# Kernel optimization log

Hardware: AMD Instinct MI355X
Metric: run time of the kernel (lower is better)

The kernel has to match this reference:

```python
import jax, jax.numpy as jnp
import numpy as np
from jax.tree_util import tree_map

B, T, D = 2, 4096, 1024
C = 512            # chunk_size
P = 16             # n_persistent
H = 2048           # neural-memory hidden
FFN = 4 * D        # ffn_mult * d_model
LR, BETA, ALPHA = 0.01, 0.9, 0.01   # memory lr / momentum / decay
EPS_LN = 1e-5


def _l2norm(x):
    n = jnp.sqrt(jnp.sum(x * x, axis=-1, keepdims=True))
    return x / jnp.maximum(n, 1e-12)


def _ln(x, g, b):
    m = jnp.mean(x, axis=-1, keepdims=True)
    v = jnp.mean((x - m) ** 2, axis=-1, keepdims=True)
    return (x - m) * jax.lax.rsqrt(v + EPS_LN) * g + b


def _mem_mlp(mem, x):
    h = jax.nn.silu(x @ mem['w0'] + mem['b0'])
    return h @ mem['w1'] + mem['b1']


def setup_inputs() -> dict:
    key = jax.random.key(0)
    ks = iter(jax.random.split(key, 32))
    w = lambda *s: jax.random.normal(next(ks), s, jnp.float32) * 0.02
    return dict(
        x=jax.random.normal(next(ks), (B, T, D), jnp.float32),
        wq_ctx=w(D, D), wq=w(D, D), wk=w(D, D), wv=w(D, D),
        w_attn_out=w(D, D), w_gate=w(D, D),
        gate_g=jnp.ones(D), gate_b=jnp.zeros(D),
        n1_g=jnp.ones(D), n1_b=jnp.zeros(D),
        n2_g=jnp.ones(D), n2_b=jnp.zeros(D),
        ffn_w1=w(D, FFN), ffn_b1=jnp.zeros(FFN),
        ffn_w2=w(FFN, D), ffn_b2=jnp.zeros(D),
        pers=w(P, D),
        mem_w0=w(D, H), mem_b0=jnp.zeros(H),
        mem_w1=w(H, D), mem_b1=jnp.zeros(D),
        mem_wk=w(D, D), mem_wv=w(D, D),
    )


def reference(x, wq_ctx, wq, wk, wv, w_attn_out, w_gate, gate_g, gate_b,
              n1_g, n1_b, n2_g, n2_b, ffn_w1, ffn_b1, ffn_w2, ffn_b2,
              pers, mem_w0, mem_b0, mem_w1, mem_b1, mem_wk, mem_wv):
    Bv, Tv, Dv = x.shape
    n_chunks = Tv // C
    scale = Dv ** 0.5
    S = P + 2 * C   # persistent + retrieved-memory tokens + segment
    # prefix-aware causal mask: i attends to j if j < P (persistent prefix) or j <= i
    ii = jnp.arange(S)[:, None]
    jj = jnp.arange(S)[None, :]
    mask = (jj < P) | (jj <= ii)                      # (S, S)

    mem0 = dict(w0=mem_w0, b0=mem_b0, w1=mem_w1, b1=mem_b1)
    mom0 = tree_map(jnp.zeros_like, mem0)

    def attn(seq):                                    # cosine causal attention, single head
        q = _l2norm(seq @ wq) * scale
        k = _l2norm(seq @ wk)
        v = seq @ wv
        scores = jnp.einsum('bqd,bkd->bqk', q, k)
        scores = jnp.where(mask, scores, -jnp.inf)
        a = jax.nn.softmax(scores, axis=-1)
        return jnp.einsum('bqk,bkd->bqd', a, v) @ w_attn_out

    def step(carry, seg):                             # seg: (B, C, D)
        mem, mom = carry
        h = _mem_mlp(mem, _l2norm(seg @ wq_ctx))      # memory retrieval, (B, C, D)
        aug = jnp.concatenate(
            [jnp.broadcast_to(pers, (Bv, P, Dv)), h, seg], axis=1)  # (B, S, D)
        y_aug = aug + attn(_ln(aug, n1_g, n1_b))
        y_t = y_aug[:, P + C:, :]                     # strip persistent, keep last C

        # surprise-gradient memory update with momentum + decay
        kk = y_t @ mem_wk
        vv = y_t @ mem_wv
        loss = lambda m: 0.5 * jnp.sum((_mem_mlp(m, kk) - vv) ** 2) / (Bv * C)
        g = jax.grad(loss)(mem)
        mom = tree_map(lambda m_, g_: BETA * m_ + g_, mom, g)
        mem = tree_map(lambda p_, m_: (1.0 - ALPHA) * p_ - LR * m_, mem, mom)

        mem_out = _mem_mlp(mem, _l2norm(y_t @ wq_ctx))
        gate = jax.nn.sigmoid(_ln(y_t, gate_g, gate_b) @ w_gate)
        o = y_t * gate + mem_out * (1.0 - gate)
        h2 = _ln(o, n2_g, n2_b)
        o = o + (jax.nn.silu(h2 @ ffn_w1 + ffn_b1) @ ffn_w2 + ffn_b2)
        return (mem, mom), o

    x_chunks = x.reshape(Bv, n_chunks, C, Dv).transpose(1, 0, 2, 3)
    _, outs = jax.lax.scan(step, (mem0, mom0), x_chunks)   # (n_chunks, B, C, D)
    return outs.transpose(1, 0, 2, 3).reshape(Bv, Tv, Dv)
```

## Files before the change

### kernel.cpp

```cpp
#include <hip/hip_runtime.h>

#define DD 1024
#define HH 2048
#define TT 4096
#define CC 512
#define PPc 16
#define SB 1040
#define KA 1088
#define FFd 4096
#define NCH 8

typedef _Float16 f16x8 __attribute__((ext_vector_type(8)));
typedef float f32x4 __attribute__((ext_vector_type(4)));

typedef const __attribute__((address_space(1))) _Float16* gas_t;
typedef __attribute__((address_space(3))) _Float16* las_t;

__device__ __forceinline__ void async_cp16(const _Float16* g, _Float16* l) {
    __builtin_amdgcn_global_load_lds((gas_t)g, (las_t)l, 16, 0, 0);
}

template<int N> __device__ __forceinline__ void waitvm() {
    static_assert(N == 0 || N == 2 || N == 3 || N == 4 || N == 6 || N == 8, "unsupported vmcnt");
    if constexpr (N == 0)      asm volatile("s_waitcnt vmcnt(0)" ::: "memory");
    else if constexpr (N == 2) asm volatile("s_waitcnt vmcnt(2)" ::: "memory");
    else if constexpr (N == 3) asm volatile("s_waitcnt vmcnt(3)" ::: "memory");
    else if constexpr (N == 4) asm volatile("s_waitcnt vmcnt(4)" ::: "memory");
    else if constexpr (N == 6) asm volatile("s_waitcnt vmcnt(6)" ::: "memory");
    else                       asm volatile("s_waitcnt vmcnt(8)" ::: "memory");
}
#define BARRIER() asm volatile("s_barrier" ::: "memory")

struct GP {
    const _Float16* A; long bsA, ldA;
    const _Float16* Bt; long bsB, ldB;
    const float* bias;
    const float* resid; long ldr, bsR;
    const float* aux;   long ldx, bsX;
    float* Cf; long ldc, bsC;
    _Float16* Ch; long ldh, bsH;
    _Float16* Ct; long ldt, bsT;
    float* Mom;
    float* Cf2;
    float s1, s2;
    int M, N, K, act;
};

template<int BM, int BN>
__global__ __launch_bounds__(256) void gemm16(GP g)
{
    constexpr int WM = BM / 2, WN = BN / 2;
    constexpr int FA = WM / 16, FB = WN / 16;
    constexpr int LA = BM / 32, LB = BN / 32;
    constexpr int LL = LA + LB;
    constexpr int APAN = BM * 64, BPAN = BN * 64;
    constexpr int NB = 3;
    __shared__ _Float16 smem[NB * (APAN + BPAN)];
    const int tid = threadIdx.x;

    const int gx = gridDim.x, gy = gridDim.y;
    const int nwg = gx * gy * (int)gridDim.z;
    const int orig = ((int)blockIdx.z * gy + (int)blockIdx.y) * gx + (int)blockIdx.x;
    const int xcd = orig & 7, loc = orig >> 3;
    const int q8 = nwg >> 3, r8 = nwg & 7;
    const int lid = (xcd < r8 ? xcd * (q8 + 1) : r8 * (q8 + 1) + (xcd - r8) * q8) + loc;
    const int bxi = lid % gx;
    const int rem = lid / gx;
    const int byi = rem % gy;
    const int z = rem / gy;

    const int K = g.K;
    const long ldA = g.ldA, ldB = g.ldB;
    const int m0 = byi * BM, n0 = bxi * BN;
    const _Float16* Ab = g.A + (long)z * g.bsA + (long)m0 * ldA;
    const _Float16* Bb = g.Bt + (long)z * g.bsB + (long)n0 * ldB;
    const int wave = tid >> 6, lane = tid & 63;
    const int wr = wave >> 1, wc = wave & 1;
    const int fr = lane & 15, kq = lane >> 4;
    const int srow = tid >> 3;
    const int sc8 = (((tid & 7) ^ (srow & 7)) << 3);
    f32x4 acc[FA][FB] = {};

    auto stage = [&](int q, int kk) {
#pragma unroll
        for (int r = 0; r < LA; ++r)
            async_cp16(Ab + (long)(r * 32 + srow) * ldA + kk + sc8,
                       &smem[q * APAN + r * 2048 + wave * 512]);
#pragma unroll
        for (int r = 0; r < LB; ++r)
            async_cp16(Bb + (long)(r * 32 + srow) * ldB + kk + sc8,
                       &smem[NB * APAN + q * BPAN + r * 2048 + wave * 512]);
    };

    const int sl0 = ((kq ^ (fr & 7)) << 3);
    const int sl1 = (((4 + kq) ^ (fr & 7)) << 3);

    auto compute = [&](int q) {
        f16x8 af[2][FA], bf[2][FB];
        const int abase = q * APAN;
#pragma unroll
        for (int i = 0; i < FA; ++i) {
            const int ro = (wr * WM + i * 16 + fr) * 64;
            af[0][i] = *(const f16x8*)&smem[abase + ro + sl0];
            af[1][i] = *(const f16x8*)&smem[abase + ro + sl1];
        }
        const int bbase = NB * APAN + q * BPAN;
#pragma unroll
        for (int j = 0; j < FB; ++j) {
            const int ro = (wc * WN + j * 16 + fr) * 64;
            bf[0][j] = *(const f16x8*)&smem[bbase + ro + sl0];
            bf[1][j] = *(const f16x8*)&smem[bbase + ro + sl1];
        }
        __builtin_amdgcn_s_setprio(1);
#pragma unroll
        for (int h = 0; h < 2; ++h)
#pragma unroll
            for (int i = 0; i < FA; ++i)
#pragma unroll
                for (int j = 0; j < FB; ++j)
                    acc[i][j] = __builtin_amdgcn_mfma_f32_16x16x32_f16(af[h][i], bf[h][j], acc[i][j], 0, 0, 0);
        __builtin_amdgcn_s_setprio(0);
    };

    const int nk = K >> 6;
    stage(0, 0); stage(1, 64);
    int qc = 0, qs = 2;
    for (int t = 0; t < nk; ++t) {
        if (t + 1 < nk) waitvm<LL>(); else waitvm<0>();
        BARRIER();
        if (t + 2 < nk) stage(qs, (t + 2) << 6);
        compute(qc);
        qc = (qc == NB - 1) ? 0 : qc + 1;
        qs = (qs == NB - 1) ? 0 : qs + 1;
    }

#pragma unroll
    for (int i = 0; i < FA; ++i) {
        const int gm0 = m0 + wr * WM + i * 16 + kq * 4;
#pragma unroll
        for (int j = 0; j < FB; ++j) {
            const int gn = n0 + wc * WN + j * 16 + fr;
            if (gn >= g.N) continue;
            if (g.act == 4) {
                const int seg = gn >> 10, gl = gn & 1023;
#pragma unroll
                for (int r = 0; r < 4; ++r) {
                    const int gm = gm0 + r;
                    if (gm >= g.M) continue;
                    const float v = acc[i][j][r];
                    if (seg == 0) g.Ch[(long)gm * 1024 + gl] = (_Float16)v;
                    else if (seg == 1) g.Cf[(long)gm * 1024 + gl] = v;
                    else g.Cf2[(long)gm * 1024 + gl] = v;
                }
            } else {
                const float bv = g.bias ? g.bias[gn] : 0.f;
#pragma unroll
                for (int r = 0; r < 4; ++r) {
                    const int gm = gm0 + r;
                    if (gm >= g.M) continue;
                    const float raw = acc[i][j][r] + bv;
                    float av = raw;
                    if (g.act == 1) av = raw / (1.f + __expf(-raw));
                    else if (g.act == 2) {
                        const float a = g.aux[(long)z * g.bsX + (long)gm * g.ldx + gn];
                        const float s = 1.f / (1.f + __expf(-a));
                        av = raw * (s * (1.f + a * (1.f - s)));
                    }
                    float v = g.s1 * av;
                    if (g.resid) v += g.s2 * g.resid[(long)z * g.bsR + (long)gm * g.ldr + gn];
                    if (g.Cf) g.Cf[(long)z * g.bsC + (long)gm * g.ldc + gn] = (g.act == 1) ? raw : v;
                    if (g.Ch) g.Ch[(long)z * g.bsH + (long)gm * g.ldh + gn] = (_Float16)v;
                    acc[i][j][r] = v;
                }
            }
        }
    }

    if (g.Ct && (g.act != 4 || n0 < 1024)) {
        constexpr int TP = BM + 8;
        __syncthreads();
#pragma unroll
        for (int i = 0; i < FA; ++i) {
            const int lm = wr * WM + i * 16 + kq * 4;
#pragma unroll
            for (int j = 0; j < FB; ++j) {
                const int ln = wc * WN + j * 16 + fr;
#pragma unroll
                for (int r = 0; r < 4; ++r)
                    smem[ln * TP + lm + r] = (_Float16)acc[i][j][r];
            }
        }
        __syncthreads();
        constexpr int TPC = 256 / BN;
        constexpr int SEG = BM / TPC;
        const int ln = tid / TPC, part = tid % TPC;
        const int gn = n0 + ln;
        if (gn < g.N) {
            const int gmb = m0 + part * SEG;
            _Float16* dst = g.Ct + (long)z * g.bsT + (long)gn * g.ldt + gmb;
            const _Float16* src = &smem[ln * TP + part * SEG];
#pragma unroll
            for (int gi = 0; gi < SEG / 8; ++gi)
                if (gmb + gi * 8 < g.M)
                    *(uint4*)(dst + gi * 8) = *(const uint4*)(src + gi * 8);
        }
    }
}

__global__ void momupT_k(const float* __restrict__ dW1, float* __restrict__ mom1,
                         float* __restrict__ w1m, _Float16* __restrict__ w1row,
                         _Float16* __restrict__ w1t,
                         const float* __restrict__ dW0, float* __restrict__ mom0,
                         float* __restrict__ w0m, _Float16* __restrict__ w0t)
{
    __shared__ _Float16 t[64][65];
    const int b = blockIdx.x;
    const int tid = threadIdx.x;
    const float* dW; float* mom; float* wm; _Float16* wrow; _Float16* wT;
    int C, RT, r0, c0;
    if (b < 512) {
        dW = dW1; mom = mom1; wm = w1m; wrow = w1row; wT = w1t;
        C = 1024; RT = 2048;
        r0 = (b >> 4) << 6; c0 = (b & 15) << 6;
    } else {
        const int bb = b - 512;
        dW = dW0; mom = mom0; wm = w0m; wrow = nullptr; wT = w0t;
        C = 2048; RT = 1024;
        r0 = (bb >> 5) << 6; c0 = (bb & 31) << 6;
    }
#pragma unroll
    for (int i = 0; i < 4; ++i) {
        const int f = i * 256 + tid;
        const int rr = f >> 4;
        const int c4 = (f & 15) << 2;
        const long idx = (long)(r0 + rr) * C + c0 + c4;
        const float4 d = *(const float4*)(dW + idx);
        float4 mo = *(const float4*)(mom + idx);
        float4 w  = *(const float4*)(wm + idx);
        mo.x = 0.9f * mo.x + d.x; mo.y = 0.9f * mo.y + d.y;
        mo.z = 0.9f * mo.z + d.z; mo.w = 0.9f * mo.w + d.w;
        w.x = 0.99f * w.x - 0.01f * mo.x; w.y = 0.99f * w.y - 0.01f * mo.y;
        w.z = 0.99f * w.z - 0.01f * mo.z; w.w = 0.99f * w.w - 0.01f * mo.w;
        *(float4*)(mom + idx) = mo;
        *(float4*)(wm + idx) = w;
        const _Float16 h0 = (_Float16)w.x, h1 = (_Float16)w.y,
                       h2 = (_Float16)w.z, h3 = (_Float16)w.w;
        if (wrow) {
            wrow[idx] = h0; wrow[idx + 1] = h1;
            wrow[idx + 2] = h2; wrow[idx + 3] = h3;
        }
        t[rr][c4] = h0; t[rr][c4 + 1] = h1; t[rr][c4 + 2] = h2; t[rr][c4 + 3] = h3;
    }
    __syncthreads();
#pragma unroll
    for (int i = 0; i < 4; ++i) {
        const int f = i * 256 + tid;
        const int cc = f >> 4;
        const int rr4 = (f & 15) << 2;
        ushort4 u;
        u.x = *(const unsigned short*)&t[rr4][cc];
        u.y = *(const unsigned short*)&t[rr4 + 1][cc];
        u.z = *(const unsigned short*)&t[rr4 + 2][cc];
        u.w = *(const unsigned short*)&t[rr4 + 3][cc];
        *(ushort4*)(wT + (long)(c0 + cc) * RT + r0 + rr4) = u;
    }
}

__global__ void cvt_k(const float* __restrict__ in, _Float16* __restrict__ out, long n)
{
    long i = ((long)blockIdx.x * 256 + threadIdx.x) * 4;
    if (i >= n) return;
    const float4 v = *(const float4*)(in + i);
    out[i] = (_Float16)v.x; out[i + 1] = (_Float16)v.y;
    out[i + 2] = (_Float16)v.z; out[i + 3] = (_Float16)v.w;
}

__global__ void cvtT_k(const float* __restrict__ in, _Float16* __restrict__ out, int R, int C)
{
    __shared__ _Float16 t[64][65];
    const int c0 = blockIdx.x * 64, r0 = blockIdx.y * 64;
    const int tid = threadIdx.x;
    for (int i = 0; i < 16; ++i) {
        const int lin = i * 256 + tid;
        const int r = lin >> 6, cc = lin & 63;
        t[r][cc] = (_Float16)in[(long)(r0 + r) * C + c0 + cc];
    }
    __syncthreads();
    for (int i = 0; i < 16; ++i) {
        const int lin = i * 256 + tid;
        const int r2 = lin >> 6, c2 = lin & 63;
        out[(long)(c0 + r2) * R + r0 + c2] = t[c2][r2];
    }
}

__global__ void l2n16s_k(const float* __restrict__ in, long ld,
                         _Float16* __restrict__ out, float scale)
{
    const long row = blockIdx.x;
    const float* p = in + row * ld;
    _Float16* q = out + row * DD;
    const int t = threadIdx.x;
    float e0 = p[t], e1 = p[t + 256], e2 = p[t + 512], e3 = p[t + 768];
    __shared__ float rq[256];
    rq[t] = e0 * e0 + e1 * e1 + e2 * e2 + e3 * e3;
    __syncthreads();
    for (int k = 128; k; k >>= 1) { if (t < k) rq[t] += rq[t + k]; __syncthreads(); }
    const float f = scale / fmaxf(sqrtf(rq[0]), 1e-12f);
    q[t] = (_Float16)(e0 * f); q[t + 256] = (_Float16)(e1 * f);
    q[t + 512] = (_Float16)(e2 * f); q[t + 768] = (_Float16)(e3 * f);
}

__global__ void l2qk_k(const float* __restrict__ qk, _Float16* __restrict__ q16,
                       _Float16* __restrict__ k16)
{
    const int blk = blockIdx.x;
    const float* p; _Float16* o; float scale;
    if (blk < 1024) {
        const int b = blk >> 9, r = blk & 511;
        p = qk + (long)(b * SB + PPc + CC + r) * 2048;
        o = q16 + (long)blk * DD; scale = 32.f;
    } else {
        const int row = blk - 1024;
        p = qk + (long)row * 2048 + 1024;
        o = k16 + (long)row * DD; scale = 1.f;
    }
    const int t = threadIdx.x;
    float e0 = p[t], e1 = p[t + 256], e2 = p[t + 512], e3 = p[t + 768];
    __shared__ float rq[256];
    rq[t] = e0 * e0 + e1 * e1 + e2 * e2 + e3 * e3;
    __syncthreads();
    for (int k = 128; k; k >>= 1) { if (t < k) rq[t] += rq[t + k]; __syncthreads(); }
    const float f = scale / fmaxf(sqrtf(rq[0]), 1e-12f);
    o[t] = (_Float16)(e0 * f); o[t + 256] = (_Float16)(e1 * f);
    o[t + 512] = (_Float16)(e2 * f); o[t + 768] = (_Float16)(e3 * f);
}

__global__ void lnaug_k(const float* __restrict__ x, const float* __restrict__ pers,
                        const float* __restrict__ h, const float* __restrict__ h2,
                        const float* __restrict__ hb,
                        const float* __restrict__ g, const float* __restrict__ b,
                        _Float16* __restrict__ out, int c)
{
    const int row = blockIdx.x;
    const int bb = row / SB, i = row % SB;
    const float* p;
    const float* p2 = nullptr;
    if (i < PPc) p = pers + (long)i * DD;
    else if (i < PPc + CC) {
        const long off = (long)(bb * CC + i - PPc) * DD;
        p = h + off; p2 = h2 + off;
    }
    else p = x + (long)(bb * TT + c * CC + (i - PPc - CC)) * DD;
    _Float16* q = out + (long)row * DD;
    const int t = threadIdx.x;
    float e0 = p[t], e1 = p[t + 256], e2 = p[t + 512], e3 = p[t + 768];
    if (p2) {
        e0 += p2[t]       + hb[t];
        e1 += p2[t + 256] + hb[t + 256];
        e2 += p2[t + 512] + hb[t + 512];
        e3 += p2[t + 768] + hb[t + 768];
    }
    __shared__ float rs[256], rq[256];
    rs[t] = e0 + e1 + e2 + e3;
    rq[t] = e0 * e0 + e1 * e1 + e2 * e2 + e3 * e3;
    __syncthreads();
    for (int k = 128; k; k >>= 1) {
        if (t < k) { rs[t] += rs[t + k]; rq[t] += rq[t + k]; }
        __syncthreads();
    }
    const float mean = rs[0] * (1.f / DD);
    const float inv = rsqrtf(rq[0] * (1.f / DD) - mean * mean + 1e-5f);
    q[t]       = (_Float16)((e0 - mean) * inv * g[t]       + b[t]);
    q[t + 256] = (_Float16)((e1 - mean) * inv * g[t + 256] + b[t + 256]);
    q[t + 512] = (_Float16)((e2 - mean) * inv * g[t + 512] + b[t + 512]);
    q[t + 768] = (_Float16)((e3 - mean) * inv * g[t + 768] + b[t + 768]);
}

__global__ void softmax16_k(const float* __restrict__ sc, _Float16* __restrict__ pr)
{
    const int blk = blockIdx.x;
    const int r = blk & 511;
    const int i = PPc + CC + r;
    const float* p = sc + (long)blk * SB;
    _Float16* q = pr + (long)blk * KA;
    const int t = threadIdx.x;
    __shared__ float red[256];
    float mx = -3.0e38f;
    for (int j = t; j < SB; j += 256)
        if (j <= i) mx = fmaxf(mx, p[j]);
    red[t] = mx; __syncthreads();
    for (int k = 128; k; k >>= 1) { if (t < k) red[t] = fmaxf(red[t], red[t + k]); __syncthreads(); }
    mx = red[0]; __syncthreads();
    float sum = 0.f;
    for (int j = t; j < SB; j += 256)
        if (j <= i) sum += __expf(p[j] - mx);
    red[t] = sum; __syncthreads();
    for (int k = 128; k; k >>= 1) { if (t < k) red[t] += red[t + k]; __syncthreads(); }
    const float inv = 1.f / red[0];
    for (int j = t; j < KA; j += 256) {
        float e = 0.f;
        if (j < SB && j <= i) e = __expf(p[j] - mx) * inv;
        q[j] = (_Float16)e;
    }
}

__global__ void gateln2_k(const float* __restrict__ yt,
                          const float* __restrict__ gp, const float* __restrict__ gp2,
                          const float* __restrict__ mo, const float* __restrict__ mo2,
                          const float* __restrict__ mb,
                          const float* __restrict__ g, const float* __restrict__ b,
                          float* __restrict__ OF, _Float16* __restrict__ o16)
{
    const long row = blockIdx.x;
    const int t = threadIdx.x;
    float e[4];
    __shared__ float rs[256], rq[256];
    float ssum = 0.f, qsum = 0.f;
#pragma unroll
    for (int k = 0; k < 4; ++k) {
        const int cc = t + k * 256;
        const long idx = row * DD + cc;
        const float gv = gp[idx] + gp2[idx];
        const float mv = mo[idx] + mo2[idx] + mb[cc];
        const float s = 1.f / (1.f + __expf(-gv));
        e[k] = yt[idx] * s + mv * (1.f - s);
        OF[idx] = e[k];
        ssum += e[k]; qsum += e[k] * e[k];
    }
    rs[t] = ssum; rq[t] = qsum;
    __syncthreads();
    for (int k = 128; k; k >>= 1) {
        if (t < k) { rs[t] += rs[t + k]; rq[t] += rq[t + k]; }
        __syncthreads();
    }
    const float mean = rs[0] * (1.f / DD);
    const float inv = rsqrtf(rq[0] * (1.f / DD) - mean * mean + 1e-5f);
#pragma unroll
    for (int k = 0; k < 4; ++k) {
        const int cc = t + k * 256;
        o16[row * DD + cc] = (_Float16)((e[k] - mean) * inv * g[cc] + b[cc]);
    }
}

__global__ void tailfuse_k(const _Float16* __restrict__ rT, const _Float16* __restrict__ daT,
                           float* __restrict__ mb0, float* __restrict__ mob0,
                           float* __restrict__ mb1, float* __restrict__ mob1,
                           const float* __restrict__ qmp, _Float16* __restrict__ qm16,
                           const float* __restrict__ ytf, const float* __restrict__ gg,
                           const float* __restrict__ gb, _Float16* __restrict__ gl)
{
    const int blk = blockIdx.x;
    const int t = threadIdx.x;
    __shared__ float rs[256], rq[256];
    if (blk < 3072) {
        const _Float16* p = (blk < 1024) ? rT + (long)blk * 1024
                                         : daT + (long)(blk - 1024) * 1024;
        rs[t] = (float)p[t] + (float)p[t + 256] + (float)p[t + 512] + (float)p[t + 768];
        __syncthreads();
        for (int k = 128; k; k >>= 1) { if (t < k) rs[t] += rs[t + k]; __syncthreads(); }
        if (t == 0) {
            const float d = rs[0];
            if (blk < 1024) {
                const float m = 0.9f * mob1[blk] + d;
                mob1[blk] = m;
                mb1[blk] = 0.99f * mb1[blk] - 0.01f * m;
            } else {
                const int j = blk - 1024;
                const float m = 0.9f * mob0[j] + d;
                mob0[j] = m;
                mb0[j] = 0.99f * mb0[j] - 0.01f * m;
            }
        }
    } else if (blk < 4096) {
        const long row = blk - 3072;
        const float* p = qmp + row * DD;
        _Float16* q = qm16 + row * DD;
        float e0 = p[t], e1 = p[t + 256], e2 = p[t + 512], e3 = p[t + 768];
        rq[t] = e0 * e0 + e1 * e1 + e2 * e2 + e3 * e3;
        __syncthreads();
        for (int k = 128; k; k >>= 1) { if (t < k) rq[t] += rq[t + k]; __syncthreads(); }
        const float f = 1.f / fmaxf(sqrtf(rq[0]), 1e-12f);
        q[t] = (_Float16)(e0 * f); q[t + 256] = (_Float16)(e1 * f);
        q[t + 512] = (_Float16)(e2 * f); q[t + 768] = (_Float16)(e3 * f);
    } else {
        const long row = blk - 4096;
        const float* p = ytf + row * DD;
        _Float16* q = gl + row * DD;
        float e0 = p[t], e1 = p[t + 256], e2 = p[t + 512], e3 = p[t + 768];
        rs[t] = e0 + e1 + e2 + e3;
        rq[t] = e0 * e0 + e1 * e1 + e2 * e2 + e3 * e3;
        __syncthreads();
        for (int k = 128; k; k >>= 1) {
            if (t < k) { rs[t] += rs[t + k]; rq[t] += rq[t + k]; }
            __syncthreads();
        }
        const float mean = rs[0] * (1.f / DD);
        const float inv = rsqrtf(rq[0] * (1.f / DD) - mean * mean + 1e-5f);
        q[t]       = (_Float16)((e0 - mean) * inv * gg[t]       + gb[t]);
        q[t + 256] = (_Float16)((e1 - mean) * inv * gg[t + 256] + gb[t + 256]);
        q[t + 512] = (_Float16)((e2 - mean) * inv * gg[t + 512] + gb[t + 512]);
        q[t + 768] = (_Float16)((e3 - mean) * inv * gg[t + 768] + gb[t + 768]);
    }
}

__global__ void zero_k(float* __restrict__ p, long n)
{
    long i = (long)blockIdx.x * 256 + threadIdx.x;
    const long st = (long)gridDim.x * 256;
    for (; i < n; i += st) p[i] = 0.f;
}

extern "C" void kernel_launch(void* const* d_in, const int* in_sizes, int n_in,
                              void* d_out, int out_size, void* d_ws, size_t ws_size,
                              hipStream_t stream)
{
    const float* x          = (const float*)d_in[0];
    const float* wq_ctx     = (const float*)d_in[1];
    const float* wq         = (const float*)d_in[2];
    const float* wk         = (const float*)d_in[3];
    const float* wv         = (const float*)d_in[4];
    const float* w_attn_out = (const float*)d_in[5];
    const float* w_gate     = (const float*)d_in[6];
    const float* gate_g     = (const float*)d_in[7];
    const float* gate_b     = (const float*)d_in[8];
    const float* n1_g       = (const float*)d_in[9];
    const float* n1_b       = (const float*)d_in[10];
    const float* n2_g       = (const float*)d_in[11];
    const float* n2_b       = (const float*)d_in[12];
    const float* ffn_w1     = (const float*)d_in[13];
    const float* ffn_b1     = (const float*)d_in[14];
    const float* ffn_w2     = (const float*)d_in[15];
    const float* ffn_b2     = (const float*)d_in[16];
    const float* pers       = (const float*)d_in[17];
    const float* mem_w0_in  = (const float*)d_in[18];
    const float* mem_b0_in  = (const float*)d_in[19];
    const float* mem_w1_in  = (const float*)d_in[20];
    const float* mem_b1_in  = (const float*)d_in[21];
    const float* mem_wk     = (const float*)d_in[22];
    const float* mem_wv     = (const float*)d_in[23];
    float* out = (float*)d_out;
    (void)in_sizes; (void)n_in; (void)out_size; (void)ws_size;

    char* cur = (char*)d_ws;
    auto allocF = [&](size_t n) { float* p = (float*)cur; cur += n * 4; return p; };
    auto allocH = [&](size_t n) { _Float16* p = (_Float16*)cur; cur += n * 2; return p; };

    float* mw0   = allocF((size_t)DD * HH);
    float* mw1   = allocF((size_t)HH * DD);
    float* mb0   = allocF(HH);
    float* mb1   = allocF(DD);
    float* mom   = allocF((size_t)DD * HH * 2 + HH + DD);
    float* mom_w0 = mom, *mom_w1 = mom + (size_t)DD * HH;
    float* mom_b0 = mom_w1 + (size_t)HH * DD, *mom_b1 = mom_b0 + HH;
    float* F32A  = allocF((size_t)1024 * DD);
    float* F32B  = allocF((size_t)1024 * DD);
    float* F32C  = allocF((size_t)1024 * HH);
    float* F32QK = allocF((size_t)2112 * 2048);
    float* YTF   = allocF((size_t)1024 * DD);
    float* OF    = allocF((size_t)1024 * DD);

    _Float16* x16    = allocH((size_t)2 * TT * DD);
    _Float16* wqcT   = allocH((size_t)DD * DD);
    _Float16* wqkT   = allocH((size_t)2048 * DD);
    _Float16* wvT    = allocH((size_t)DD * DD);
    _Float16* waoT   = allocH((size_t)DD * DD);
    _Float16* wgT    = allocH((size_t)DD * DD);
    _Float16* wmixT  = allocH((size_t)3072 * DD);
    _Float16* f1T    = allocH((size_t)FFd * DD);
    _Float16* f2T    = allocH((size_t)DD * FFd);
    _Float16* w0T    = allocH((size_t)HH * DD);
    _Float16* w1T    = allocH((size_t)DD * HH);
    _Float16* w1p    = allocH((size_t)HH * DD);
    _Float16* xn16   = allocH((size_t)1024 * DD);
    _Float16* h116   = allocH((size_t)1024 * HH);
    _Float16* laug16 = allocH((size_t)2208 * DD);
    _Float16* q16    = allocH((size_t)1024 * DD);
    _Float16* k16    = allocH((size_t)2208 * DD);
    _Float16* vT16   = allocH((size_t)2 * DD * KA);
    _Float16* pr16   = allocH((size_t)2 * 512 * KA);
    _Float16* ao16   = allocH((size_t)1024 * DD);
    _Float16* yt16   = allocH((size_t)1024 * DD);
    _Float16* kk16   = allocH((size_t)1024 * DD);
    _Float16* kkT16  = allocH((size_t)DD * 1024);
    _Float16* hs16   = allocH((size_t)1024 * HH);
    _Float16* hsT16  = allocH((size_t)HH * 1024);
    _Float16* r16    = allocH((size_t)1024 * DD);
    _Float16* rT16   = allocH((size_t)DD * 1024);
    _Float16* da0T   = allocH((size_t)HH * 1024);
    _Float16* qm16   = allocH((size_t)1024 * DD);
    _Float16* a216   = allocH((size_t)1024 * HH);
    _Float16* gl16   = allocH((size_t)1024 * DD);
    _Float16* h216   = allocH((size_t)1024 * DD);
    _Float16* f116   = allocH((size_t)1024 * FFd);

    float* SPL0 = F32QK;
    float* SPL1 = F32QK + (size_t)1024 * 1024;

    auto launch = [&](int nz, GP g) {
        if (!g.ldA) g.ldA = g.K;
        if (!g.ldB) g.ldB = g.K;
        dim3 grid((g.N + 63) / 64, (g.M + 63) / 64, nz);
        gemm16<64, 64><<<grid, 256, 0, stream>>>(g);
    };

    hipMemcpyAsync(mw0, mem_w0_in, sizeof(float) * DD * HH, hipMemcpyDeviceToDevice, stream);
    hipMemcpyAsync(mw1, mem_w1_in, sizeof(float) * HH * DD, hipMemcpyDeviceToDevice, stream);
    hipMemcpyAsync(mb0, mem_b0_in, sizeof(float) * HH, hipMemcpyDeviceToDevice, stream);
    hipMemcpyAsync(mb1, mem_b1_in, sizeof(float) * DD, hipMemcpyDeviceToDevice, stream);
    zero_k<<<4096, 256, 0, stream>>>(mom, (long)DD * HH * 2 + HH + DD);
    cvt_k<<<(2 * TT * DD) / 1024, 256, 0, stream>>>(x, x16, (long)2 * TT * DD);
    auto T64 = [&](const float* in, _Float16* o, int R, int C) {
        cvtT_k<<<dim3(C / 64, R / 64), 256, 0, stream>>>(in, o, R, C);
    };
    T64(wq_ctx, wqcT, DD, DD);
    T64(wq, wqkT, DD, DD); T64(wk, wqkT + (size_t)1024 * DD, DD, DD);
    T64(wv, wvT, DD, DD); T64(w_attn_out, waoT, DD, DD); T64(w_gate, wgT, DD, DD);
    T64(mem_wk, wmixT, DD, DD); T64(mem_wv, wmixT + (size_t)1024 * DD, DD, DD);
    T64(wq_ctx, wmixT + (size_t)2048 * DD, DD, DD);
    T64(ffn_w1, f1T, DD, FFd); T64(ffn_w2, f2T, FFd, DD);
    T64(mem_w0_in, w0T, DD, HH); T64(mem_w1_in, w1T, HH, DD);
    cvt_k<<<(HH * DD) / 1024, 256, 0, stream>>>(mem_w1_in, w1p, (long)HH * DD);

    for (int c = 0; c < NCH; ++c) {
        GP g;
        g = GP{}; g.A = x16 + (long)c * CC * DD; g.bsA = (long)TT * DD; g.Bt = wqcT;
        g.Cf = F32A; g.ldc = DD; g.bsC = (long)CC * DD;
        g.s1 = 1.f; g.M = CC; g.N = DD; g.K = DD;
        launch(2, g);
        l2n16s_k<<<1024, 256, 0, stream>>>(F32A, DD, xn16, 1.f);
        g = GP{}; g.A = xn16; g.Bt = w0T; g.bias = mb0; g.Ch = h116; g.ldh = HH;
        g.s1 = 1.f; g.M = 1024; g.N = HH; g.K = DD; g.act = 1;
        launch(1, g);
        g = GP{}; g.A = h116; g.bsA = 1024; g.ldA = HH;
        g.Bt = w1T; g.bsB = 1024; g.ldB = HH;
        g.Cf = F32B; g.ldc = DD; g.bsC = (long)(SPL0 - F32B);
        g.s1 = 1.f; g.M = 1024; g.N = DD; g.K = 1024;
        launch(2, g);
        lnaug_k<<<2 * SB, 256, 0, stream>>>(x, pers, F32B, SPL0, mb1, n1_g, n1_b, laug16, c);
        g = GP{}; g.A = laug16; g.Bt = wqkT; g.Cf = F32QK; g.ldc = 2048;
        g.s1 = 1.f; g.M = 2 * SB; g.N = 2048; g.K = DD;
        launch(1, g);
        l2qk_k<<<3104, 256, 0, stream>>>(F32QK, q16, k16);
        g = GP{}; g.A = laug16; g.bsA = (long)SB * DD; g.Bt = wvT;
        g.Ct = vT16; g.ldt = KA; g.bsT = (long)DD * KA;
        g.s1 = 1.f; g.M = SB; g.N = DD; g.K = DD;
        launch(2, g);
        g = GP{}; g.A = q16; g.bsA = (long)512 * DD; g.Bt = k16; g.bsB = (long)SB * DD;
        g.Cf = F32C; g.ldc = SB; g.bsC = (long)512 * SB;
        g.s1 = 1.f; g.M = 512; g.N = SB; g.K = DD;
        launch(2, g);
        softmax16_k<<<1024, 256, 0, stream>>>(F32C, pr16);
        g = GP{}; g.A = pr16; g.bsA = (long)512 * KA; g.Bt = vT16; g.bsB = (long)DD * KA;
        g.Ch = ao16; g.ldh = DD; g.bsH = (long)512 * DD;
        g.s1 = 1.f; g.M = 512; g.N = DD; g.K = KA;
        launch(2, g);
        g = GP{}; g.A = ao16; g.bsA = (long)512 * DD; g.Bt = waoT;
        g.resid = x + (long)c * CC * DD; g.ldr = DD; g.bsR = (long)TT * DD;
        g.Cf = YTF; g.ldc = DD; g.bsC = (long)512 * DD;
        g.Ch = yt16; g.ldh = DD; g.bsH = (long)512 * DD;
        g.s1 = 1.f; g.s2 = 1.f; g.M = 512; g.N = DD; g.K = DD;
        launch(2, g);
        g = GP{}; g.A = yt16; g.Bt = wmixT; g.Ch = kk16; g.Ct = kkT16; g.ldt = 1024;
        g.Cf = F32B; g.Cf2 = F32A;
        g.s1 = 1.f; g.M = 1024; g.N = 3072; g.K = DD; g.act = 4;
        launch(1, g);
        g = GP{}; g.A = kk16; g.Bt = w0T; g.bias = mb0; g.Cf = F32C; g.ldc = HH;
        g.Ch = hs16; g.ldh = HH; g.Ct = hsT16; g.ldt = 1024;
        g.s1 = 1.f; g.M = 1024; g.N = HH; g.K = DD; g.act = 1;
        launch(1, g);
        g = GP{}; g.A = hs16; g.Bt = w1T; g.bias = mb1;
        g.resid = F32B; g.ldr = DD;
        g.Ch = r16; g.ldh = DD; g.Ct = rT16; g.ldt = 1024;
        g.s1 = 1.f / 1024.f; g.s2 = -1.f / 1024.f; g.M = 1024; g.N = DD; g.K = HH;
        launch(1, g);
        g = GP{}; g.A = r16; g.Bt = w1p; g.aux = F32C; g.ldx = HH;
        g.Ct = da0T; g.ldt = 1024;
        g.s1 = 1.f; g.M = 1024; g.N = HH; g.K = DD; g.act = 2;
        launch(1, g);
        tailfuse_k<<<5120, 256, 0, stream>>>(rT16, da0T, mb0, mom_b0, mb1, mom_b1,
                                             F32A, qm16, YTF, gate_g, gate_b, gl16);
        g = GP{}; g.A = hsT16; g.Bt = rT16; g.Cf = F32C; g.ldc = DD;
        g.s1 = 1.f; g.M = HH; g.N = DD; g.K = 1024;
        launch(1, g);
        g = GP{}; g.A = kkT16; g.Bt = da0T; g.Cf = F32QK; g.ldc = HH;
        g.s1 = 1.f; g.M = DD; g.N = HH; g.K = 1024;
        launch(1, g);
        momupT_k<<<1024, 256, 0, stream>>>(F32C, mom_w1, mw1, w1p, w1T,
                                           F32QK, mom_w0, mw0, w0T);
        g = GP{}; g.A = qm16; g.Bt = w0T; g.bias = mb0; g.Ch = a216; g.ldh = HH;
        g.s1 = 1.f; g.M = 1024; g.N = HH; g.K = DD; g.act = 1;
        launch(1, g);
        g = GP{}; g.A = a216; g.bsA = 1024; g.ldA = HH;
        g.Bt = w1T; g.bsB = 1024; g.ldB = HH;
        g.Cf = F32B; g.ldc = DD; g.bsC = (long)(SPL0 - F32B);
        g.s1 = 1.f; g.M = 1024; g.N = DD; g.K = 1024;
        launch(2, g);
        g = GP{}; g.A = gl16; g.bsA = 512; g.ldA = DD;
        g.Bt = wgT; g.bsB = 512; g.ldB = DD;
        g.Cf = F32C; g.ldc = DD; g.bsC = (long)(SPL1 - F32C);
        g.s1 = 1.f; g.M = 1024; g.N = DD; g.K = 512;
        launch(2, g);
        gateln2_k<<<1024, 256, 0, stream>>>(YTF, F32C, SPL1, F32B, SPL0, mb1,
                                            n2_g, n2_b, OF, h216);
        g = GP{}; g.A = h216; g.Bt = f1T; g.bias = ffn_b1; g.Ch = f116; g.ldh = FFd;
        g.s1 = 1.f; g.M = 1024; g.N = FFd; g.K = DD; g.act = 1;
        launch(1, g);
        g = GP{}; g.A = f116; g.bsA = (long)512 * FFd; g.Bt = f2T; g.bias = ffn_b2;
        g.resid = OF; g.ldr = DD; g.bsR = (long)512 * DD;
        g.Cf = out + (long)c * CC * DD; g.ldc = DD; g.bsC = (long)TT * DD;
        g.s1 = 1.f; g.s2 = 1.f; g.M = 512; g.N = DD; g.K = FFd;
        launch(2, g);
    }
}
```

Baseline: 3.039 ms.

## Hoist context-query projection out of chunk loop and split-K the FFN down-projection

The retrieval query projection x@wq_ctx and its l2-norm depend only on the input, so they are now computed once for all tokens before the chunk loop instead of once per chunk. The FFN second GEMM (K=4096, M=512 per batch) is split into two K-halves written to separate fp32 buffers, and a new kernel sums them with bias and residual into the output. This gives the long-K GEMM more blocks to fill the GPU, at the cost of extra fp32 traffic and one more launch. The kk^T·da0 result is moved to a different offset in F32QK so it does not overlap SPL0/SPL1.

New measurement: 2.880 ms. 5.2% less time.

```diff
diff --git a/kernel.cpp b/kernel.cpp
--- a/kernel.cpp
+++ b/kernel.cpp
@@ -439,6 +439,22 @@
     for (int k = 0; k < 4; ++k) {
         const int cc = t + k * 256;
         o16[row * DD + cc] = (_Float16)((e[k] - mean) * inv * g[cc] + b[cc]);
+    }
+}
+
+__global__ void ffnout_k(const float* __restrict__ h0, const float* __restrict__ h1,
+                         const float* __restrict__ bias, const float* __restrict__ OF,
+                         float* __restrict__ out, int c)
+{
+    const int row = blockIdx.x;
+    const int b = row >> 9, rr = row & 511;
+    const int t = threadIdx.x;
+    const long src = (long)row * DD;
+    float* o = out + (long)b * TT * DD + (long)(c * CC + rr) * DD;
+#pragma unroll
+    for (int k = 0; k < 4; ++k) {
+        const int cc = t + k * 256;
+        o[cc] = h0[src + cc] + h1[src + cc] + bias[cc] + OF[src + cc];
     }
 }
 
@@ -571,7 +587,7 @@
     _Float16* w0T    = allocH((size_t)HH * DD);
     _Float16* w1T    = allocH((size_t)DD * HH);
     _Float16* w1p    = allocH((size_t)HH * DD);
-    _Float16* xn16   = allocH((size_t)1024 * DD);
+    _Float16* xn16   = allocH((size_t)2 * TT * DD);
     _Float16* h116   = allocH((size_t)1024 * HH);
     _Float16* laug16 = allocH((size_t)2208 * DD);
     _Float16* q16    = allocH((size_t)1024 * DD);
@@ -595,6 +611,7 @@
 
     float* SPL0 = F32QK;
     float* SPL1 = F32QK + (size_t)1024 * 1024;
+    float* XN = F32C;
 
     auto launch = [&](int nz, GP g) {
         if (!g.ldA) g.ldA = g.K;
@@ -621,16 +638,19 @@
     T64(mem_w0_in, w0T, DD, HH); T64(mem_w1_in, w1T, HH, DD);
     cvt_k<<<(HH * DD) / 1024, 256, 0, stream>>>(mem_w1_in, w1p, (long)HH * DD);
 
+    {
+        GP g{}; g.A = x16; g.Bt = wqcT; g.Cf = XN; g.ldc = DD;
+        g.s1 = 1.f; g.M = 2 * TT; g.N = DD; g.K = DD;
+        launch(1, g);
+        l2n16s_k<<<2 * TT, 256, 0, stream>>>(XN, DD, xn16, 1.f);
+    }
+
     for (int c = 0; c < NCH; ++c) {
         GP g;
-        g = GP{}; g.A = x16 + (long)c * CC * DD; g.bsA = (long)TT * DD; g.Bt = wqcT;
-        g.Cf = F32A; g.ldc = DD; g.bsC = (long)CC * DD;
-        g.s1 = 1.f; g.M = CC; g.N = DD; g.K = DD;
-        launch(2, g);
-        l2n16s_k<<<1024, 256, 0, stream>>>(F32A, DD, xn16, 1.f);
-        g = GP{}; g.A = xn16; g.Bt = w0T; g.bias = mb0; g.Ch = h116; g.ldh = HH;
-        g.s1 = 1.f; g.M = 1024; g.N = HH; g.K = DD; g.act = 1;
-        launch(1, g);
+        g = GP{}; g.A = xn16 + (long)c * CC * DD; g.bsA = (long)TT * DD;
+        g.Bt = w0T; g.bias = mb0; g.Ch = h116; g.ldh = HH; g.bsH = (long)CC * HH;
+        g.s1 = 1.f; g.M = CC; g.N = HH; g.K = DD; g.act = 1;
+        launch(2, g);
         g = GP{}; g.A = h116; g.bsA = 1024; g.ldA = HH;
         g.Bt = w1T; g.bsB = 1024; g.ldB = HH;
         g.Cf = F32B; g.ldc = DD; g.bsC = (long)(SPL0 - F32B);
@@ -682,11 +702,11 @@
         g = GP{}; g.A = hsT16; g.Bt = rT16; g.Cf = F32C; g.ldc = DD;
         g.s1 = 1.f; g.M = HH; g.N = DD; g.K = 1024;
         launch(1, g);
-        g = GP{}; g.A = kkT16; g.Bt = da0T; g.Cf = F32QK; g.ldc = HH;
+        g = GP{}; g.A = kkT16; g.Bt = da0T; g.Cf = F32QK + (size_t)2048 * 1024; g.ldc = HH;
         g.s1 = 1.f; g.M = DD; g.N = HH; g.K = 1024;
         launch(1, g);
         momupT_k<<<1024, 256, 0, stream>>>(F32C, mom_w1, mw1, w1p, w1T,
-                                           F32QK, mom_w0, mw0, w0T);
+                                           F32QK + (size_t)2048 * 1024, mom_w0, mw0, w0T);
         g = GP{}; g.A = qm16; g.Bt = w0T; g.bias = mb0; g.Ch = a216; g.ldh = HH;
         g.s1 = 1.f; g.M = 1024; g.N = HH; g.K = DD; g.act = 1;
         launch(1, g);
@@ -705,10 +725,12 @@
         g = GP{}; g.A = h216; g.Bt = f1T; g.bias = ffn_b1; g.Ch = f116; g.ldh = FFd;
         g.s1 = 1.f; g.M = 1024; g.N = FFd; g.K = DD; g.act = 1;
         launch(1, g);
-        g = GP{}; g.A = f116; g.bsA = (long)512 * FFd; g.Bt = f2T; g.bias = ffn_b2;
-        g.resid = OF; g.ldr = DD; g.bsR = (long)512 * DD;
-        g.Cf = out + (long)c * CC * DD; g.ldc = DD; g.bsC = (long)TT * DD;
-        g.s1 = 1.f; g.s2 = 1.f; g.M = 512; g.N = DD; g.K = FFd;
-        launch(2, g);
-    }
-}
+        g = GP{}; g.A = f116; g.bsA = 2048; g.ldA = FFd;
+        g.Bt = f2T; g.bsB = 2048; g.ldB = FFd;
+        g.Cf = F32B; g.ldc = DD; g.bsC = (long)(SPL0 - F32B);
+        g.s1 = 1.f; g.M = 1024; g.N = DD; g.K = 2048;
+        launch(2, g);
+        ffnout_k<<<1024, 256, 0, stream>>>(F32B, SPL0, ffn_b2, OF,
+                                           out, c);
+    }
+}
```
